# Optimization experiments

Hardware: AMD Instinct MI355X
Metric: run time of the kernel (lower is better)

Reference implementation:

```python
import jax, jax.numpy as jnp
import numpy as np

IN, H, OUT, T = 512, 2048, 512, 8192


def setup_inputs() -> dict:
    key = jax.random.key(0)
    ks = jax.random.split(key, 9)
    s = 1.0 / np.sqrt(H).astype(np.float32)  # PyTorch LSTM/Linear init range
    u = lambda k, shape: jax.random.uniform(k, shape, jnp.float32, -s, s)
    return {
        "sequence": jax.random.normal(ks[0], (T, IN), jnp.float32),
        "W_ih": u(ks[1], (4 * H, IN)),
        "W_hh": u(ks[2], (4 * H, H)),
        "b_ih": u(ks[3], (4 * H,)),
        "b_hh": u(ks[4], (4 * H,)),
        "h0": jax.random.normal(ks[5], (H,), jnp.float32),  # module's random hidden init (batch=1 flattened)
        "c0": jax.random.normal(ks[6], (H,), jnp.float32),
        "W_lin": u(ks[7], (OUT, H)),
        "b_lin": u(ks[8], (OUT,)),
    }


def reference(sequence, W_ih, W_hh, b_ih, b_hh, h0, c0, W_lin, b_lin):
    # Precompute input contribution to gates for all timesteps in one GEMM: [T, 4H]
    x_gates = sequence @ W_ih.T + (b_ih + b_hh)

    def cell(carry, xg):
        h, c = carry
        g = xg + h @ W_hh.T                      # [4H]
        i, f, gg, o = jnp.split(g, 4)            # PyTorch gate order: i, f, g, o
        i = jax.nn.sigmoid(i)
        f = jax.nn.sigmoid(f)
        gg = jnp.tanh(gg)
        o = jax.nn.sigmoid(o)
        c = f * c + i * gg
        h = o * jnp.tanh(c)
        return (h, c), h

    (h_last, _), _ = jax.lax.scan(cell, (h0, c0), x_gates)
    # linear on every step then take last == linear on last hidden state
    pred = h_last @ W_lin.T + b_lin              # [OUT]
    return pred[None, :]                          # [1, OUT], matches prediction[-1]
```

## Files before the change

### kernel.cpp

```cpp
#include <hip/hip_runtime.h>
#include <hip/hip_bf16.h>
#include <stdint.h>



__device__ __forceinline__ uint32_t packf16(float a, float b) {
    auto h = __builtin_amdgcn_cvt_pkrtz(a, b);
    return __builtin_bit_cast(uint32_t, h);
}

__device__ __forceinline__ float dot2h(uint32_t a, uint32_t b, float c) {
    float d;
    asm("v_dot2_f32_f16 %0, %1, %2, %3" : "=v"(d) : "v"(a), "v"(b), "v"(c));
    return d;
}

template <int CTRL>
__device__ __forceinline__ float movdpp(float x) {
    return __int_as_float(__builtin_amdgcn_mov_dpp(__float_as_int(x), CTRL, 0xF, 0xF, true));
}

__device__ __forceinline__ float xorsum16(float x) {
#if __has_builtin(__builtin_amdgcn_permlane16_swap)
    auto r = __builtin_amdgcn_permlane16_swap(__float_as_uint(x), __float_as_uint(x), false, false);
    return __uint_as_float(r[0]) + __uint_as_float(r[1]);
#else
    return x + __shfl_xor(x, 16, 64);
#endif
}

__device__ __forceinline__ float xorsum32(float x) {
#if __has_builtin(__builtin_amdgcn_permlane32_swap)
    auto r = __builtin_amdgcn_permlane32_swap(__float_as_uint(x), __float_as_uint(x), false, false);
    return __uint_as_float(r[0]) + __uint_as_float(r[1]);
#else
    return x + __shfl_xor(x, 32, 64);
#endif
}

__device__ __forceinline__ float sigm(float x) { return 1.f / (1.f + __expf(-x)); }
__device__ __forceinline__ float tanh_fast(float x) { return 1.f - 2.f / (1.f + __expf(2.f * x)); }

#define ASTORE(p, v) __hip_atomic_store((p), (v), __ATOMIC_RELAXED, __HIP_MEMORY_SCOPE_AGENT)

__device__ __forceinline__ void poll_issue(const unsigned long long* pa,
                                           const unsigned long long* pb,
                                           ulonglong2& ra, ulonglong2& rb) {
    asm volatile(
        "global_load_dwordx4 %0, %2, off sc0 sc1\n\t"
        "global_load_dwordx4 %1, %3, off sc0 sc1"
        : "=v"(ra), "=v"(rb)
        : "v"(pa), "v"(pb)
        : "memory");
    __builtin_amdgcn_sched_barrier(0);
}

__device__ __forceinline__ void poll_wait() {
    asm volatile("s_waitcnt vmcnt(0)" ::: "memory");
    __builtin_amdgcn_sched_barrier(0);
}

__global__ __launch_bounds__(256) void init_hbuf(unsigned long long* hbuf) {
    int i = blockIdx.x * 256 + threadIdx.x;
    if (i < 2048) hbuf[i] = ~0ull;
}

__global__ __launch_bounds__(256, 1) void lstm_persist(const float* __restrict__ seq,
                                                       const float* __restrict__ Wih,
                                                       const float* __restrict__ Whh,
                                                       const float* __restrict__ bih,
                                                       const float* __restrict__ bhh,
                                                       const float* __restrict__ h0,
                                                       const float* __restrict__ c0,
                                                       unsigned long long* hbuf,
                                                       float* __restrict__ hf32) {
    const int b = blockIdx.x, tid = threadIdx.x;
    const int q = tid >> 6, lane = tid & 63;
    const int hb = b * 8;
    const int rb = (lane >> 2) & 1;
    const int myrow = hb + 2 * q + rb;

    uint32_t w[160];
#pragma unroll
    for (int c = 0; c < 8; c++) {
        const int R = (c >> 1) * 2048 + hb + 2 * q + (c & 1);
        const float2* rih = (const float2*)(Wih + (size_t)R * 512);
        const float2* rhh = (const float2*)(Whh + (size_t)R * 2048);
#pragma unroll
        for (int k = 0; k < 4; k++) {
            float2 v = rih[k * 64 + lane];
            w[c * 20 + k] = packf16(v.x, v.y);
        }
#pragma unroll
        for (int j = 0; j < 4; j++)
#pragma unroll
            for (int i = 0; i < 4; i++) {
                float2 v = rhh[256 * j + 4 * lane + i];
                w[c * 20 + 4 + 4 * j + i] = packf16(v.x, v.y);
            }
    }

    __shared__ alignas(16) uint32_t v_stage[2][1024];

    const float bi  = bih[myrow] + bhh[myrow];
    const float bf_ = bih[2048 + myrow] + bhh[2048 + myrow];
    const float bg  = bih[4096 + myrow] + bhh[4096 + myrow];
    const float bo  = bih[6144 + myrow] + bhh[6144 + myrow];
    float c_state = c0[myrow];

    if (q == 0 && lane < 4) {
        float a = h0[hb + lane * 2], b2 = h0[hb + lane * 2 + 1];
        unsigned long long v = ((unsigned long long)packf16(a, b2) << 32);
        ASTORE(&hbuf[b * 4 + lane], v);
    }

    float2 xn[4];
#pragma unroll
    for (int k = 0; k < 4; k++) xn[k] = ((const float2*)seq)[k * 64 + lane];

    int gave_up = 0;

    for (int s = 1; s <= 8192; s++) {
        const int t = s - 1, bs = t & 1;
        const uint32_t want = (uint32_t)t;

        uint32_t x0 = packf16(xn[0].x, xn[0].y), x1 = packf16(xn[1].x, xn[1].y);
        uint32_t x2 = packf16(xn[2].x, xn[2].y), x3 = packf16(xn[3].x, xn[3].y);
        __builtin_amdgcn_sched_barrier(0);

        const unsigned long long* base = hbuf + (bs << 10) + q * 256;
        const unsigned long long* pa = base + 2 * lane;
        const unsigned long long* pb = base + 128 + 2 * lane;
        ulonglong2 ra, rb2;
        poll_issue(pa, pb, ra, rb2);

        float acc[8];
#pragma unroll
        for (int c = 0; c < 8; c++) {
            float a = dot2h(w[c * 20 + 0], x0, 0.f);
            a = dot2h(w[c * 20 + 1], x1, a);
            a = dot2h(w[c * 20 + 2], x2, a);
            acc[c] = dot2h(w[c * 20 + 3], x3, a);
        }

        if (!gave_up) {
            int tries = 0;
            for (;;) {
                poll_wait();
                int ok = ((uint32_t)ra.x == want) & ((uint32_t)ra.y == want) &
                         ((uint32_t)rb2.x == want) & ((uint32_t)rb2.y == want);
                if (__all(ok)) break;
                if (++tries > (1 << 17)) { gave_up = 1; break; }
                poll_issue(pa, pb, ra, rb2);
                if (tries > 2) __builtin_amdgcn_s_sleep(1);
            }
        } else {
            poll_wait();
        }

        {
            uint2* vsa = (uint2*)&v_stage[bs][q * 256 + 2 * lane];
            uint2* vsb = (uint2*)&v_stage[bs][q * 256 + 128 + 2 * lane];
            *vsa = make_uint2((uint32_t)(ra.x >> 32), (uint32_t)(ra.y >> 32));
            *vsb = make_uint2((uint32_t)(rb2.x >> 32), (uint32_t)(rb2.y >> 32));
        }

        __syncthreads();

        if (s < 8192) {
            const float2* xp = (const float2*)(seq + (size_t)s * 512);
#pragma unroll
            for (int k = 0; k < 4; k++) xn[k] = xp[k * 64 + lane];
        }

#pragma unroll
        for (int j = 0; j < 4; j++) {
            const uint4 hv = *(const uint4*)&v_stage[bs][256 * j + 4 * lane];
#pragma unroll
            for (int c = 0; c < 8; c++) {
                float a = dot2h(w[c * 20 + 4 + 4 * j + 0], hv.x, acc[c]);
                a = dot2h(w[c * 20 + 4 + 4 * j + 1], hv.y, a);
                a = dot2h(w[c * 20 + 4 + 4 * j + 2], hv.z, a);
                acc[c] = dot2h(w[c * 20 + 4 + 4 * j + 3], hv.w, a);
            }
        }

#pragma unroll
        for (int j = 0; j < 4; j++) {
            float lo = acc[j], hi = acc[j + 4];
            float sel = (lane & 1) ? lo : hi;
            float got = movdpp<0xB1>(sel);
            acc[j] = ((lane & 1) ? hi : lo) + got;
        }
#pragma unroll
        for (int j = 0; j < 2; j++) {
            float lo = acc[j], hi = acc[j + 2];
            float sel = (lane & 2) ? lo : hi;
            float got = movdpp<0x4E>(sel);
            acc[j] = ((lane & 2) ? hi : lo) + got;
        }
        {
            float lo = acc[0], hi = acc[1];
            float sel = (lane & 4) ? lo : hi;
            float got = __shfl_xor(sel, 4, 64);
            acc[0] = ((lane & 4) ? hi : lo) + got;
        }
        acc[0] += movdpp<0x128>(acc[0]);
        acc[0] = xorsum16(acc[0]);
        acc[0] = xorsum32(acc[0]);

        float gi = movdpp<0x00>(acc[0]);
        float gg = movdpp<0x55>(acc[0]);
        float gf = movdpp<0xAA>(acc[0]);
        float go = movdpp<0xFF>(acc[0]);
        float i_ = sigm(gi + bi), f_ = sigm(gf + bf_), g_ = tanh_fast(gg + bg), o_ = sigm(go + bo);
        c_state = f_ * c_state + i_ * g_;
        float hval = o_ * tanh_fast(c_state);

        float h1 = movdpp<0x124>(hval);
        if (lane == 0) {
            unsigned long long v = ((unsigned long long)packf16(hval, h1) << 32) | (uint32_t)s;
            ASTORE(&hbuf[((s & 1) << 10) + b * 4 + q], v);
            if (s == 8192) { hf32[hb + 2 * q] = hval; hf32[hb + 2 * q + 1] = h1; }
        }
    }
}

__global__ __launch_bounds__(256) void final_linear(const float* __restrict__ hf,
                                                    const float* __restrict__ Wlin,
                                                    const float* __restrict__ blin,
                                                    float* __restrict__ out) {
    const int row = blockIdx.x * 4 + (threadIdx.x >> 6);
    const int lane = threadIdx.x & 63;
    float acc = 0.f;
#pragma unroll
    for (int it = 0; it < 8; it++) {
        int c = it * 256 + lane * 4;
        float4 wv = *(const float4*)&Wlin[(size_t)row * 2048 + c];
        float4 hv = *(const float4*)&hf[c];
        acc += wv.x * hv.x + wv.y * hv.y + wv.z * hv.z + wv.w * hv.w;
    }
#pragma unroll
    for (int off = 32; off; off >>= 1) acc += __shfl_xor(acc, off, 64);
    if (lane == 0) out[row] = acc + blin[row];
}

extern "C" void kernel_launch(void* const* d_in, const int* in_sizes, int n_in,
                              void* d_out, int out_size, void* d_ws, size_t ws_size,
                              hipStream_t stream) {
    const float* seq  = (const float*)d_in[0];
    const float* Wih  = (const float*)d_in[1];
    const float* Whh  = (const float*)d_in[2];
    const float* bih  = (const float*)d_in[3];
    const float* bhh  = (const float*)d_in[4];
    const float* h0   = (const float*)d_in[5];
    const float* c0   = (const float*)d_in[6];
    const float* Wlin = (const float*)d_in[7];
    const float* blin = (const float*)d_in[8];
    float* out = (float*)d_out;

    char* ws = (char*)d_ws;
    unsigned long long* hbuf = (unsigned long long*)ws;
    float* hf32 = (float*)(ws + 16384);

    init_hbuf<<<8, 256, 0, stream>>>(hbuf);
    lstm_persist<<<256, 256, 0, stream>>>(seq, Wih, Whh, bih, bhh, h0, c0, hbuf, hf32);
    final_linear<<<128, 256, 0, stream>>>(hf32, Wlin, blin, out);
}
```

Measured before the change: 14.35 ms.

## Replace per-step workgroup barrier with per-wave LDS flags and rotated consumption

Removes the __syncthreads after each wave stages its quarter of the hidden vector in LDS. Each wave now publishes a step-stamped LDS flag, starts its dot products on its own quarter, and spins on the other waves' flags in rotated order. The goal is to overlap a wave's compute with the others' global polling and cut barrier stalls on the recurrent critical path. The cost is extra spin loads and reliance on acquire/release ordering in LDS, with a bounded spin that could race if ordering is wrong. Summation order now differs per wave, so results may change slightly.

```diff
diff --git a/kernel.cpp b/kernel.cpp
--- a/kernel.cpp
+++ b/kernel.cpp
@@ -42,6 +42,8 @@
 __device__ __forceinline__ float tanh_fast(float x) { return 1.f - 2.f / (1.f + __expf(2.f * x)); }
 
 #define ASTORE(p, v) __hip_atomic_store((p), (v), __ATOMIC_RELAXED, __HIP_MEMORY_SCOPE_AGENT)
+#define LDS_ST(p, v) __hip_atomic_store((p), (v), __ATOMIC_RELAXED, __HIP_MEMORY_SCOPE_WORKGROUP)
+#define LDS_LDACQ(p) __hip_atomic_load((p), __ATOMIC_ACQUIRE, __HIP_MEMORY_SCOPE_WORKGROUP)
 
 __device__ __forceinline__ void poll_issue(const unsigned long long* pa,
                                            const unsigned long long* pb,
@@ -101,6 +103,8 @@
     }
 
     __shared__ alignas(16) uint32_t v_stage[2][1024];
+    __shared__ alignas(16) uint32_t qflag[2][4];
+    if (tid < 8) ((uint32_t*)qflag)[tid] = 0;
 
     const float bi  = bih[myrow] + bhh[myrow];
     const float bf_ = bih[2048 + myrow] + bhh[2048 + myrow];
@@ -118,7 +122,31 @@
 #pragma unroll
     for (int k = 0; k < 4; k++) xn[k] = ((const float2*)seq)[k * 64 + lane];
 
+    __syncthreads();
+
     int gave_up = 0;
+
+#define HQ_WAIT(jj)                                                                       \
+    {                                                                                     \
+        uint32_t fj = LDS_LDACQ(&qflag[bs][(jj)]);                                        \
+        if (fj != su) {                                                                   \
+            int zz = 0;                                                                   \
+            do { fj = LDS_LDACQ(&qflag[bs][(jj)]); } while (fj != su && ++zz < (1 << 20)); \
+        }                                                                                 \
+        __builtin_amdgcn_sched_barrier(0);                                                \
+    }
+
+#define HQ_DOT(jj)                                                                        \
+    {                                                                                     \
+        const uint4 hv = *(const uint4*)&v_stage[bs][256 * (jj) + 4 * lane];              \
+        _Pragma("unroll")                                                                 \
+        for (int c = 0; c < 8; c++) {                                                     \
+            float a = dot2h(w[c * 20 + 4 + 4 * (jj) + 0], hv.x, acc[c]);                  \
+            a = dot2h(w[c * 20 + 4 + 4 * (jj) + 1], hv.y, a);                             \
+            a = dot2h(w[c * 20 + 4 + 4 * (jj) + 2], hv.z, a);                             \
+            acc[c] = dot2h(w[c * 20 + 4 + 4 * (jj) + 3], hv.w, a);                        \
+        }                                                                                 \
+    }
 
     for (int s = 1; s <= 8192; s++) {
         const int t = s - 1, bs = t & 1;
@@ -163,9 +191,10 @@
             uint2* vsb = (uint2*)&v_stage[bs][q * 256 + 128 + 2 * lane];
             *vsa = make_uint2((uint32_t)(ra.x >> 32), (uint32_t)(ra.y >> 32));
             *vsb = make_uint2((uint32_t)(rb2.x >> 32), (uint32_t)(rb2.y >> 32));
-        }
-
-        __syncthreads();
+            asm volatile("s_waitcnt lgkmcnt(0)" ::: "memory");
+            __builtin_amdgcn_sched_barrier(0);
+            if (lane == 0) LDS_ST(&qflag[bs][q], (uint32_t)s);
+        }
 
         if (s < 8192) {
             const float2* xp = (const float2*)(seq + (size_t)s * 512);
@@ -173,16 +202,15 @@
             for (int k = 0; k < 4; k++) xn[k] = xp[k * 64 + lane];
         }
 
-#pragma unroll
-        for (int j = 0; j < 4; j++) {
-            const uint4 hv = *(const uint4*)&v_stage[bs][256 * j + 4 * lane];
-#pragma unroll
-            for (int c = 0; c < 8; c++) {
-                float a = dot2h(w[c * 20 + 4 + 4 * j + 0], hv.x, acc[c]);
-                a = dot2h(w[c * 20 + 4 + 4 * j + 1], hv.y, a);
-                a = dot2h(w[c * 20 + 4 + 4 * j + 2], hv.z, a);
-                acc[c] = dot2h(w[c * 20 + 4 + 4 * j + 3], hv.w, a);
-            }
+        const uint32_t su = (uint32_t)s;
+        if (q == 0) {
+            HQ_DOT(0); HQ_WAIT(1) HQ_DOT(1); HQ_WAIT(2) HQ_DOT(2); HQ_WAIT(3) HQ_DOT(3);
+        } else if (q == 1) {
+            HQ_DOT(1); HQ_WAIT(2) HQ_DOT(2); HQ_WAIT(3) HQ_DOT(3); HQ_WAIT(0) HQ_DOT(0);
+        } else if (q == 2) {
+            HQ_DOT(2); HQ_WAIT(3) HQ_DOT(3); HQ_WAIT(0) HQ_DOT(0); HQ_WAIT(1) HQ_DOT(1);
+        } else {
+            HQ_DOT(3); HQ_WAIT(0) HQ_DOT(0); HQ_WAIT(1) HQ_DOT(1); HQ_WAIT(2) HQ_DOT(2);
         }
 
 #pragma unroll
@@ -224,6 +252,8 @@
             if (s == 8192) { hf32[hb + 2 * q] = hval; hf32[hb + 2 * q + 1] = h1; }
         }
     }
+#undef HQ_WAIT
+#undef HQ_DOT
 }
 
 __global__ __launch_bounds__(256) void final_linear(const float* __restrict__ hf,
```

Measured after the change: 24.04 ms. 1.68x slower.
